# Kernel optimization log

Hardware: AMD Instinct MI355X
Metric: run time of the kernel (lower is better)

The kernel has to match this reference:

```python
import jax, jax.numpy as jnp
import numpy as np

N = 100000          # nodes
E = 1600000         # edges
D_NODE = 128        # num_node_features
D_EDGE = 128        # num_edge_features
OUT = 64            # out_features
HEADS = 2
HID = OUT * HEADS   # 128
NUM_GRAPHS = 64
NEG_SLOPE = 0.2


def setup_inputs() -> dict:
    key = jax.random.key(0)
    ks = jax.random.split(key, 12)
    glorot = lambda k, shape: jax.random.uniform(
        k, shape, jnp.float32, -1.0, 1.0) * np.sqrt(6.0 / (shape[0] + shape[-1]))
    return {
        "x": jax.random.normal(ks[0], (N, D_NODE), jnp.float32),
        "edge_index": jax.random.randint(ks[1], (2, E), 0, N, jnp.int64),
        "edge_attr": jax.random.normal(ks[2], (E, D_EDGE), jnp.float32),
        "batch": jnp.sort(jax.random.randint(ks[3], (N,), 0, NUM_GRAPHS, jnp.int64)),
        # GATConv params
        "lin_w": glorot(ks[4], (D_NODE, HID)),
        "att_src": glorot(ks[5], (HEADS, OUT)),
        "att_dst": glorot(ks[6], (HEADS, OUT)),
        "gat_bias": jnp.zeros((HID,), jnp.float32),
        # edge_lin params
        "edge_w": glorot(ks[7], (D_EDGE, HID)),
        "edge_b": jnp.zeros((HID,), jnp.float32),
        # MLP params
        "w1": glorot(ks[8], (HID, 32)),
        "b1": jnp.zeros((32,), jnp.float32),
        "w2": glorot(ks[9], (32, 1)),
        "b2": jnp.zeros((1,), jnp.float32),
    }


def reference(x, edge_index, edge_attr, batch, lin_w, att_src, att_dst,
              gat_bias, edge_w, edge_b, w1, b1, w2, b2):
    n = x.shape[0]
    # --- GATConv (concat=True, add_self_loops=True, negative_slope=0.2) ---
    h = (x @ lin_w).reshape(n, HEADS, OUT)                 # [N,H,C]
    loop = jnp.arange(n, dtype=edge_index.dtype)
    src = jnp.concatenate([edge_index[0], loop])           # [E+N]
    dst = jnp.concatenate([edge_index[1], loop])
    a_src = jnp.sum(h * att_src, axis=-1)                  # [N,H]
    a_dst = jnp.sum(h * att_dst, axis=-1)
    e = jax.nn.leaky_relu(a_src[src] + a_dst[dst], NEG_SLOPE)  # [E+N,H]
    e_max = jax.ops.segment_max(e, dst, num_segments=n)    # softmax over incoming edges
    e_exp = jnp.exp(e - e_max[dst])
    denom = jax.ops.segment_sum(e_exp, dst, num_segments=n)
    alpha = e_exp / (denom[dst] + 1e-16)                   # [E+N,H]
    msg = h[src] * alpha[:, :, None]                       # [E+N,H,C]
    node_feat = jax.ops.segment_sum(msg, dst, num_segments=n)
    node_feat = node_feat.reshape(n, HID) + gat_bias       # [N,HID]
    # --- edge features: linear + scatter-add to SOURCE node (the python loop) ---
    edge_feat = edge_attr @ edge_w + edge_b                # [E,HID]
    edge_agg = jax.ops.segment_sum(edge_feat, edge_index[0], num_segments=n)
    combined = node_feat + edge_agg                        # [N,HID]
    # --- global_add_pool + MLP ---
    pooled = jax.ops.segment_sum(combined, batch, num_segments=NUM_GRAPHS)
    return (pooled @ w1 + b1) @ w2 + b2                    # [NUM_GRAPHS,1]
```

## Files before the change

### kernel.cpp

```cpp
#include <hip/hip_runtime.h>
#include <hip/hip_bf16.h>
#include <math.h>


#define NG 64

__device__ __forceinline__ float lrelu(float v){ return v > 0.f ? v : 0.2f*v; }

__global__ __launch_bounds__(256) void k_zero(float4* __restrict__ p, long long n4,
                                              int* __restrict__ nstart)
{
  long long i = (long long)blockIdx.x*256 + threadIdx.x;
  long long stride = (long long)gridDim.x*256;
  float4 z = make_float4(0.f,0.f,0.f,0.f);
  for (; i < n4; i += stride) p[i] = z;
  if (blockIdx.x == 0 && threadIdx.x < NG) nstart[threadIdx.x] = 0x7fffffff;
}

__global__ __launch_bounds__(256) void k_gemm_h(
    const float* __restrict__ x, const float* __restrict__ W,
    const float* __restrict__ att_src, const float* __restrict__ att_dst,
    float* __restrict__ h, float* __restrict__ aS, float* __restrict__ aD,
    float* __restrict__ denom, int N)
{
  __shared__ float ldsX[32*128];
  int rb = blockIdx.x * 32;
  for (int idx = threadIdx.x; idx < 32*128/4; idx += 256){
    int k = (idx*4) & 127;
    int row = rb + (idx >> 5);
    float4 v = make_float4(0.f,0.f,0.f,0.f);
    if (row < N) v = *(const float4*)&x[(size_t)row*128 + k];
    *(float4*)&ldsX[idx*4] = v;
  }
  __syncthreads();
  int ty = threadIdx.x >> 5, tx = threadIdx.x & 31;
  int r0 = ty*4, c0 = tx*4;
  float acc[4][4] = {};
  #pragma unroll 4
  for (int k = 0; k < 128; ++k){
    float4 b = *(const float4*)&W[k*128 + c0];
    float a0 = ldsX[(r0+0)*128 + k];
    float a1 = ldsX[(r0+1)*128 + k];
    float a2 = ldsX[(r0+2)*128 + k];
    float a3 = ldsX[(r0+3)*128 + k];
    acc[0][0] += a0*b.x; acc[0][1] += a0*b.y; acc[0][2] += a0*b.z; acc[0][3] += a0*b.w;
    acc[1][0] += a1*b.x; acc[1][1] += a1*b.y; acc[1][2] += a1*b.z; acc[1][3] += a1*b.w;
    acc[2][0] += a2*b.x; acc[2][1] += a2*b.y; acc[2][2] += a2*b.z; acc[2][3] += a2*b.w;
    acc[3][0] += a3*b.x; acc[3][1] += a3*b.y; acc[3][2] += a3*b.z; acc[3][3] += a3*b.w;
  }
  #pragma unroll
  for (int i=0;i<4;++i){
    int row = rb + r0 + i;
    if (row < N){
      float4 v = make_float4(acc[i][0],acc[i][1],acc[i][2],acc[i][3]);
      *(float4*)&h[(size_t)row*128 + c0] = v;
    }
  }
  float4 vs = *(const float4*)&att_src[c0];
  float4 vd = *(const float4*)&att_dst[c0];
  int head = tx >> 4;
  #pragma unroll
  for (int i=0;i<4;++i){
    float ps = acc[i][0]*vs.x + acc[i][1]*vs.y + acc[i][2]*vs.z + acc[i][3]*vs.w;
    float pd = acc[i][0]*vd.x + acc[i][1]*vd.y + acc[i][2]*vd.z + acc[i][3]*vd.w;
    ps += __shfl_xor(ps,1); ps += __shfl_xor(ps,2); ps += __shfl_xor(ps,4); ps += __shfl_xor(ps,8);
    pd += __shfl_xor(pd,1); pd += __shfl_xor(pd,2); pd += __shfl_xor(pd,4); pd += __shfl_xor(pd,8);
    if ((tx & 15) == 0){
      int row = rb + r0 + i;
      if (row < N){
        aS[row*2+head] = ps;
        aD[row*2+head] = pd;
        denom[row*2+head] = __expf(lrelu(ps+pd));
      }
    }
  }
}

__global__ __launch_bounds__(256) void k_deg_denom(
  const int* __restrict__ src, const int* __restrict__ dst,
  const float* __restrict__ aS, const float* __restrict__ aD,
  int* __restrict__ deg, float* __restrict__ denom, int E)
{
  int e = blockIdx.x*256 + threadIdx.x; if (e >= E) return;
  int s = src[e], d = dst[e];
  atomicAdd(&deg[s], 1);
  float2 as = *(const float2*)&aS[(size_t)s*2];
  float2 ad = *(const float2*)&aD[(size_t)d*2];
  atomicAdd(&denom[d*2+0], __expf(lrelu(as.x+ad.x)));
  atomicAdd(&denom[d*2+1], __expf(lrelu(as.y+ad.y)));
}

__global__ __launch_bounds__(256) void k_bsum(
  const int* __restrict__ deg, int* __restrict__ bsum, int N)
{
  __shared__ int s[256];
  int b = blockIdx.x, t = threadIdx.x, base = b*1024;
  int sum = 0;
  #pragma unroll
  for (int q=0;q<4;++q){ int i = base + t*4 + q; if (i < N) sum += deg[i]; }
  s[t] = sum; __syncthreads();
  for (int o=128;o;o>>=1){ if (t<o) s[t]+=s[t+o]; __syncthreads(); }
  if (t==0) bsum[b] = s[0];
}

__global__ void k_bscan(const int* __restrict__ bsum, int* __restrict__ boff,
                        int* __restrict__ doff, int nbk, int N, int E)
{
  if (threadIdx.x == 0){
    int s = 0;
    for (int b=0;b<nbk;++b){ boff[b]=s; s+=bsum[b]; }
    doff[N] = E;
  }
}

__global__ __launch_bounds__(256) void k_doff(
  const int* __restrict__ deg, const int* __restrict__ boff,
  int* __restrict__ doff, int* __restrict__ gpos, int N)
{
  __shared__ int s[256];
  int b = blockIdx.x, t = threadIdx.x, base = b*1024;
  int v[4]; int t4 = 0;
  #pragma unroll
  for (int q=0;q<4;++q){ int i = base + t*4 + q; v[q] = (i<N)?deg[i]:0; t4 += v[q]; }
  s[t] = t4; __syncthreads();
  for (int o=1;o<256;o<<=1){
    int add = (t>=o)? s[t-o] : 0;
    __syncthreads();
    s[t] += add;
    __syncthreads();
  }
  int run = boff[b] + s[t] - t4;
  #pragma unroll
  for (int q=0;q<4;++q){
    int i = base + t*4 + q;
    if (i < N){ doff[i] = run; gpos[i] = run; run += v[q]; }
  }
}

__global__ __launch_bounds__(256) void k_node_post(
  const float* __restrict__ aD, const float* __restrict__ denom,
  const int* __restrict__ batch, float4* __restrict__ adn,
  int* __restrict__ nstart, int N)
{
  int i = blockIdx.x*256 + threadIdx.x; if (i >= N) return;
  adn[i] = make_float4(aD[i*2], aD[i*2+1], denom[i*2], denom[i*2+1]);
  int b = batch[i];
  if (i == 0 || batch[i-1] != b) atomicMin(&nstart[b], i);
}

__global__ void k_bounds(const int* __restrict__ nstart, const int* __restrict__ doff,
                         int N, int E, int* __restrict__ goff_e,
                         float* __restrict__ cnt_nf, float* __restrict__ cnt_ef)
{
  if (threadIdx.x != 0) return;
  int arr[NG+1];
  arr[NG] = N;
  for (int g=NG-1; g>=0; --g){
    int v = nstart[g];
    arr[g] = (v <= N) ? v : arr[g+1];
  }
  for (int g=0; g<NG; ++g) goff_e[g] = doff[arr[g]];
  goff_e[NG] = E;
  for (int g=0; g<NG; ++g){
    cnt_nf[g] = (float)(arr[g+1]-arr[g]);
    cnt_ef[g] = (float)(goff_e[g+1]-goff_e[g]);
  }
}

__global__ __launch_bounds__(256) void k_scatter(
  const int* __restrict__ src, const int* __restrict__ dst,
  int* __restrict__ gpos, int2* __restrict__ order2, int E)
{
  int e = blockIdx.x*256 + threadIdx.x; if (e >= E) return;
  int s = src[e];
  int p = atomicAdd(&gpos[s], 1);
  order2[p] = make_int2(e, dst[e] | ((s & 63) << 17));
}

__global__ __launch_bounds__(256) void k_alpha_rows(
  const int2* __restrict__ order2, const int* __restrict__ doff,
  const float* __restrict__ aS, const float4* __restrict__ adn,
  const int* __restrict__ batch, float* __restrict__ P, int N)
{
  __shared__ float row[64*128];
  __shared__ float saS[128];
  __shared__ int sb[64];
  int s0 = blockIdx.x*64, t = threadIdx.x;
  for (int idx=t; idx<2048; idx+=256) ((float4*)row)[idx] = make_float4(0,0,0,0);
  if (t < 128){ int i = s0*2 + t; saS[t] = (i < 2*N) ? aS[i] : 0.f; }
  if (t < 64){ int i = s0 + t; sb[t] = (i < N) ? batch[i] : 0; }
  __syncthreads();
  int hi = s0 + 64; if (hi > N) hi = N;
  int i0 = doff[s0], i1 = doff[hi];
  for (int i = i0 + t; i < i1; i += 256){
    int y = order2[i].y;
    int d = y & 0x1FFFF;
    int lo = (y >> 17) & 63;
    float4 q = adn[d];
    int gb = batch[d];
    float a0 = __expf(lrelu(saS[lo*2+0] + q.x)) / (q.z + 1e-16f);
    float a1 = __expf(lrelu(saS[lo*2+1] + q.y)) / (q.w + 1e-16f);
    atomicAdd(&row[lo*128 + gb],      a0);
    atomicAdd(&row[lo*128 + 64 + gb], a1);
  }
  __syncthreads();
  if (t < 64){
    int s = s0 + t;
    if (s < N){
      float4 q = adn[s];
      row[t*128 + sb[t]]      += __expf(lrelu(saS[t*2+0] + q.x)) / (q.z + 1e-16f);
      row[t*128 + 64 + sb[t]] += __expf(lrelu(saS[t*2+1] + q.y)) / (q.w + 1e-16f);
    }
  }
  __syncthreads();
  for (int idx=t; idx<2048; idx+=256){
    int r = idx >> 5;
    int s = s0 + r;
    if (s < N) ((float4*)&P[(size_t)s*128])[idx & 31] = ((float4*)row)[idx];
  }
}

__global__ __launch_bounds__(256) void k_pgemm(
  const float* __restrict__ P, const float* __restrict__ h,
  float* __restrict__ partial, int N)
{
  __shared__ float sP[64*128];
  int t = threadIdx.x;
  int c = t & 127;
  int gh = t >> 7;
  int head = c >> 6;
  float acc[32];
  #pragma unroll
  for (int i=0;i<32;++i) acc[i] = 0.f;
  int j0 = blockIdx.x * 256;
  for (int sbi=0; sbi<4; ++sbi){
    int jb = j0 + sbi*64;
    __syncthreads();
    for (int idx=t; idx<2048; idx+=256){
      int j = jb + (idx >> 5);
      ((float4*)sP)[idx] = (j < N) ? ((const float4*)&P[(size_t)j*128])[idx & 31]
                                   : make_float4(0,0,0,0);
    }
    __syncthreads();
    for (int jj=0; jj<64; ++jj){
      int j = jb + jj;
      float hv = (j < N) ? h[(size_t)j*128 + c] : 0.f;
      const float* rp = &sP[jj*128 + head*64 + gh*32];
      #pragma unroll
      for (int q=0;q<8;++q){
        float4 pv = *(const float4*)&rp[q*4];
        acc[q*4+0] += pv.x*hv; acc[q*4+1] += pv.y*hv;
        acc[q*4+2] += pv.z*hv; acc[q*4+3] += pv.w*hv;
      }
    }
  }
  float* pb = &partial[(size_t)blockIdx.x*8192];
  #pragma unroll
  for (int i=0;i<32;++i) pb[(gh*32+i)*128 + c] = acc[i];
}

__global__ __launch_bounds__(256) void k_pg_reduce(
  const float* __restrict__ partial, float* __restrict__ pooled_gat, int nPB)
{
  int o = blockIdx.x*256 + threadIdx.x;
  float s = 0.f;
  for (int b=0; b<nPB; ++b) s += partial[(size_t)b*8192 + o];
  pooled_gat[o] = s;
}

#define EA_SPLITS 64
__global__ __launch_bounds__(256) void k_eattr_sum(
  const float* __restrict__ ea, const int2* __restrict__ order2,
  const int* __restrict__ goff_e, float* __restrict__ pooled_e)
{
  __shared__ int sord[512];
  __shared__ float facc[128];
  int g = blockIdx.x / EA_SPLITS, k = blockIdx.x % EA_SPLITS;
  int start = goff_e[g], cnt = goff_e[g+1] - start;
  int len = (cnt + EA_SPLITS - 1) / EA_SPLITS;
  int i0 = start + k*len;
  int i1 = start + cnt; if (i0 + len < i1) i1 = i0 + len;
  int t = threadIdx.x, lane = t & 31, sub = t >> 5;
  const float4* ea4 = (const float4*)ea;
  float4 acc = make_float4(0.f,0.f,0.f,0.f);
  for (int base = i0; base < i1; base += 512){
    int m = i1 - base; if (m > 512) m = 512;
    __syncthreads();
    for (int idx = t; idx < m; idx += 256) sord[idx] = order2[base + idx].x;
    __syncthreads();
    int j = sub;
    for (; j + 56 < m; j += 64){
      float4 v0 = ea4[(size_t)sord[j     ]*32 + lane];
      float4 v1 = ea4[(size_t)sord[j +  8]*32 + lane];
      float4 v2 = ea4[(size_t)sord[j + 16]*32 + lane];
      float4 v3 = ea4[(size_t)sord[j + 24]*32 + lane];
      float4 v4 = ea4[(size_t)sord[j + 32]*32 + lane];
      float4 v5 = ea4[(size_t)sord[j + 40]*32 + lane];
      float4 v6 = ea4[(size_t)sord[j + 48]*32 + lane];
      float4 v7 = ea4[(size_t)sord[j + 56]*32 + lane];
      acc.x += (v0.x+v1.x)+(v2.x+v3.x)+((v4.x+v5.x)+(v6.x+v7.x));
      acc.y += (v0.y+v1.y)+(v2.y+v3.y)+((v4.y+v5.y)+(v6.y+v7.y));
      acc.z += (v0.z+v1.z)+(v2.z+v3.z)+((v4.z+v5.z)+(v6.z+v7.z));
      acc.w += (v0.w+v1.w)+(v2.w+v3.w)+((v4.w+v5.w)+(v6.w+v7.w));
    }
    for (; j < m; j += 8){
      float4 v = ea4[(size_t)sord[j]*32 + lane];
      acc.x += v.x; acc.y += v.y; acc.z += v.z; acc.w += v.w;
    }
  }
  if (t < 128) facc[t] = 0.f;
  __syncthreads();
  float* a = &facc[lane*4];
  atomicAdd(a+0, acc.x); atomicAdd(a+1, acc.y);
  atomicAdd(a+2, acc.z); atomicAdd(a+3, acc.w);
  __syncthreads();
  if (t < 128) atomicAdd(&pooled_e[g*128 + t], facc[t]);
}

__global__ __launch_bounds__(128) void k_final(
  const float* __restrict__ pooled_gat, const float* __restrict__ pooled_e,
  const float* __restrict__ cnt_nf, const float* __restrict__ cnt_ef,
  const float* __restrict__ gat_bias, const float* __restrict__ edge_w,
  const float* __restrict__ edge_b, const float* __restrict__ w1,
  const float* __restrict__ b1, const float* __restrict__ w2,
  const float* __restrict__ b2, float* __restrict__ out)
{
  __shared__ float lds_e[128], comb[128], t1[32];
  int g = blockIdx.x, c = threadIdx.x;
  lds_e[c] = pooled_e[g*128 + c];
  __syncthreads();
  float acc = pooled_gat[g*128 + c] + cnt_nf[g]*gat_bias[c] + cnt_ef[g]*edge_b[c];
  for (int k=0; k<128; ++k) acc += lds_e[k] * edge_w[k*128 + c];
  comb[c] = acc;
  __syncthreads();
  if (c < 32){
    float tv = b1[c];
    for (int k=0; k<128; ++k) tv += comb[k] * w1[k*32 + c];
    t1[c] = tv;
  }
  __syncthreads();
  if (c == 0){
    float o = b2[0];
    #pragma unroll
    for (int m=0; m<32; ++m) o += t1[m] * w2[m];
    out[g] = o;
  }
}

extern "C" void kernel_launch(void* const* d_in, const int* in_sizes, int n_in,
                              void* d_out, int out_size, void* d_ws, size_t ws_size,
                              hipStream_t stream) {
  const float* x        = (const float*)d_in[0];
  const int*   ei       = (const int*)d_in[1];
  const float* ea       = (const float*)d_in[2];
  const int*   batch    = (const int*)d_in[3];
  const float* lin_w    = (const float*)d_in[4];
  const float* att_src  = (const float*)d_in[5];
  const float* att_dst  = (const float*)d_in[6];
  const float* gat_bias = (const float*)d_in[7];
  const float* edge_w   = (const float*)d_in[8];
  const float* edge_b   = (const float*)d_in[9];
  const float* w1       = (const float*)d_in[10];
  const float* b1       = (const float*)d_in[11];
  const float* w2       = (const float*)d_in[12];
  const float* b2       = (const float*)d_in[13];
  float* out = (float*)d_out;

  int N = in_sizes[0] / 128;
  int E = in_sizes[1] / 2;
  const int* src = ei;
  const int* dst = ei + E;
  int nbk = (N + 1023) / 1024;
  int nPB = (N + 255) / 256;

  char* ws = (char*)d_ws;
  size_t off = 0;
  float* pooled_e   = (float*)(ws + off); off += (size_t)NG*128*4;
  int*   deg        = (int*)  (ws + off); off += ((size_t)N*4 + 15) & ~15ull;
  size_t zero_bytes = off;
  float* pooled_gat = (float*)(ws + off); off += (size_t)NG*128*4;
  float* h        = (float*)(ws + off); off += (size_t)N*128*4;
  float* P        = (float*)(ws + off); off += (size_t)N*128*4;
  float* partial  = (float*)(ws + off); off += (size_t)nPB*8192*4;
  float* aS       = (float*)(ws + off); off += (size_t)2*N*4;
  float* aD       = (float*)(ws + off); off += (size_t)2*N*4;
  float* denom    = (float*)(ws + off); off += (size_t)2*N*4;
  float4* adn     = (float4*)(ws + off); off += (size_t)N*16;
  int*   doff     = (int*)  (ws + off); off += ((size_t)(N+1)*4 + 15) & ~15ull;
  int*   gpos     = (int*)  (ws + off); off += ((size_t)N*4 + 15) & ~15ull;
  int2*  order2   = (int2*) (ws + off); off += (size_t)E*8;
  int*   bsum     = (int*)  (ws + off); off += 1024*4;
  int*   boff     = (int*)  (ws + off); off += 1024*4;
  int*   nstart   = (int*)  (ws + off); off += NG*4;
  int*   goff_e   = (int*)  (ws + off); off += (NG+1)*4;
  float* cnt_nf   = (float*)(ws + off); off += NG*4;
  float* cnt_ef   = (float*)(ws + off); off += NG*4;

  k_zero<<<128, 256, 0, stream>>>((float4*)d_ws, (long long)(zero_bytes/16), nstart);

  k_gemm_h   <<<(N+31)/32, 256, 0, stream>>>(x, lin_w, att_src, att_dst,
                                             h, aS, aD, denom, N);
  k_deg_denom<<<(E+255)/256, 256, 0, stream>>>(src, dst, aS, aD, deg, denom, E);

  k_bsum     <<<nbk, 256, 0, stream>>>(deg, bsum, N);
  k_bscan    <<<1, 1, 0, stream>>>(bsum, boff, doff, nbk, N, E);
  k_doff     <<<nbk, 256, 0, stream>>>(deg, boff, doff, gpos, N);
  k_node_post<<<(N+255)/256, 256, 0, stream>>>(aD, denom, batch, adn, nstart, N);
  k_bounds   <<<1, 1, 0, stream>>>(nstart, doff, N, E, goff_e, cnt_nf, cnt_ef);
  k_scatter  <<<(E+255)/256, 256, 0, stream>>>(src, dst, gpos, order2, E);

  k_alpha_rows<<<(N+63)/64, 256, 0, stream>>>(order2, doff, aS, adn, batch, P, N);
  k_pgemm     <<<nPB, 256, 0, stream>>>(P, h, partial, N);
  k_pg_reduce <<<32, 256, 0, stream>>>(partial, pooled_gat, nPB);

  k_eattr_sum<<<NG*EA_SPLITS, 256, 0, stream>>>(ea, order2, goff_e, pooled_e);

  k_final<<<NG, 128, 0, stream>>>(pooled_gat, pooled_e, cnt_nf, cnt_ef,
                                  gat_bias, edge_w, edge_b, w1, b1, w2, b2, out);
}
```

Baseline: 822.2 us.

## Split edge order into SoA arrays, pack batch id, retune pgemm and reduction

The interleaved int2 edge-order buffer becomes two separate int arrays, so the alpha and edge-attribute passes each read only the field they use. The destination's graph id is packed into the order word at scatter time, which removes a random batch[] gather in k_alpha_rows. k_pgemm now covers 128 nodes per block instead of 256, giving more blocks and more parallelism, and the partial-sum reduction is split across a 2D grid that combines results with atomics into a pre-zeroed pooled_gat. The price is a doubled partial buffer that the reduce must read, plus atomic contention during the final combine.

```diff
diff --git a/kernel.cpp b/kernel.cpp
--- a/kernel.cpp
+++ b/kernel.cpp
@@ -169,16 +169,19 @@
 
 __global__ __launch_bounds__(256) void k_scatter(
   const int* __restrict__ src, const int* __restrict__ dst,
-  int* __restrict__ gpos, int2* __restrict__ order2, int E)
+  const int* __restrict__ batch, int* __restrict__ gpos,
+  int* __restrict__ order_x, int* __restrict__ order_y, int E)
 {
   int e = blockIdx.x*256 + threadIdx.x; if (e >= E) return;
-  int s = src[e];
+  int s = src[e], d = dst[e];
+  int gb = batch[d];
   int p = atomicAdd(&gpos[s], 1);
-  order2[p] = make_int2(e, dst[e] | ((s & 63) << 17));
+  order_x[p] = e;
+  order_y[p] = d | ((s & 63) << 17) | (gb << 23);
 }
 
 __global__ __launch_bounds__(256) void k_alpha_rows(
-  const int2* __restrict__ order2, const int* __restrict__ doff,
+  const int* __restrict__ order_y, const int* __restrict__ doff,
   const float* __restrict__ aS, const float4* __restrict__ adn,
   const int* __restrict__ batch, float* __restrict__ P, int N)
 {
@@ -193,11 +196,11 @@
   int hi = s0 + 64; if (hi > N) hi = N;
   int i0 = doff[s0], i1 = doff[hi];
   for (int i = i0 + t; i < i1; i += 256){
-    int y = order2[i].y;
+    int y = order_y[i];
     int d = y & 0x1FFFF;
     int lo = (y >> 17) & 63;
+    int gb = (y >> 23) & 63;
     float4 q = adn[d];
-    int gb = batch[d];
     float a0 = __expf(lrelu(saS[lo*2+0] + q.x)) / (q.z + 1e-16f);
     float a1 = __expf(lrelu(saS[lo*2+1] + q.y)) / (q.w + 1e-16f);
     atomicAdd(&row[lo*128 + gb],      a0);
@@ -232,8 +235,8 @@
   float acc[32];
   #pragma unroll
   for (int i=0;i<32;++i) acc[i] = 0.f;
-  int j0 = blockIdx.x * 256;
-  for (int sbi=0; sbi<4; ++sbi){
+  int j0 = blockIdx.x * 128;
+  for (int sbi=0; sbi<2; ++sbi){
     int jb = j0 + sbi*64;
     __syncthreads();
     for (int idx=t; idx<2048; idx+=256){
@@ -263,14 +266,17 @@
   const float* __restrict__ partial, float* __restrict__ pooled_gat, int nPB)
 {
   int o = blockIdx.x*256 + threadIdx.x;
+  int chunk = (nPB + gridDim.y - 1) / gridDim.y;
+  int b0 = blockIdx.y * chunk;
+  int b1 = b0 + chunk; if (b1 > nPB) b1 = nPB;
   float s = 0.f;
-  for (int b=0; b<nPB; ++b) s += partial[(size_t)b*8192 + o];
-  pooled_gat[o] = s;
+  for (int b=b0; b<b1; ++b) s += partial[(size_t)b*8192 + o];
+  atomicAdd(&pooled_gat[o], s);
 }
 
 #define EA_SPLITS 64
 __global__ __launch_bounds__(256) void k_eattr_sum(
-  const float* __restrict__ ea, const int2* __restrict__ order2,
+  const float* __restrict__ ea, const int* __restrict__ order_x,
   const int* __restrict__ goff_e, float* __restrict__ pooled_e)
 {
   __shared__ int sord[512];
@@ -286,7 +292,7 @@
   for (int base = i0; base < i1; base += 512){
     int m = i1 - base; if (m > 512) m = 512;
     __syncthreads();
-    for (int idx = t; idx < m; idx += 256) sord[idx] = order2[base + idx].x;
+    for (int idx = t; idx < m; idx += 256) sord[idx] = order_x[base + idx];
     __syncthreads();
     int j = sub;
     for (; j + 56 < m; j += 64){
@@ -371,14 +377,14 @@
   const int* src = ei;
   const int* dst = ei + E;
   int nbk = (N + 1023) / 1024;
-  int nPB = (N + 255) / 256;
+  int nPB = (N + 127) / 128;
 
   char* ws = (char*)d_ws;
   size_t off = 0;
   float* pooled_e   = (float*)(ws + off); off += (size_t)NG*128*4;
+  float* pooled_gat = (float*)(ws + off); off += (size_t)NG*128*4;
   int*   deg        = (int*)  (ws + off); off += ((size_t)N*4 + 15) & ~15ull;
   size_t zero_bytes = off;
-  float* pooled_gat = (float*)(ws + off); off += (size_t)NG*128*4;
   float* h        = (float*)(ws + off); off += (size_t)N*128*4;
   float* P        = (float*)(ws + off); off += (size_t)N*128*4;
   float* partial  = (float*)(ws + off); off += (size_t)nPB*8192*4;
@@ -388,7 +394,8 @@
   float4* adn     = (float4*)(ws + off); off += (size_t)N*16;
   int*   doff     = (int*)  (ws + off); off += ((size_t)(N+1)*4 + 15) & ~15ull;
   int*   gpos     = (int*)  (ws + off); off += ((size_t)N*4 + 15) & ~15ull;
-  int2*  order2   = (int2*) (ws + off); off += (size_t)E*8;
+  int*   order_x  = (int*)  (ws + off); off += (size_t)E*4;
+  int*   order_y  = (int*)  (ws + off); off += (size_t)E*4;
   int*   bsum     = (int*)  (ws + off); off += 1024*4;
   int*   boff     = (int*)  (ws + off); off += 1024*4;
   int*   nstart   = (int*)  (ws + off); off += NG*4;
@@ -407,13 +414,17 @@
   k_doff     <<<nbk, 256, 0, stream>>>(deg, boff, doff, gpos, N);
   k_node_post<<<(N+255)/256, 256, 0, stream>>>(aD, denom, batch, adn, nstart, N);
   k_bounds   <<<1, 1, 0, stream>>>(nstart, doff, N, E, goff_e, cnt_nf, cnt_ef);
-  k_scatter  <<<(E+255)/256, 256, 0, stream>>>(src, dst, gpos, order2, E);
-
-  k_alpha_rows<<<(N+63)/64, 256, 0, stream>>>(order2, doff, aS, adn, batch, P, N);
+  k_scatter  <<<(E+255)/256, 256, 0, stream>>>(src, dst, batch, gpos,
+                                               order_x, order_y, E);
+
+  k_alpha_rows<<<(N+63)/64, 256, 0, stream>>>(order_y, doff, aS, adn, batch, P, N);
   k_pgemm     <<<nPB, 256, 0, stream>>>(P, h, partial, N);
-  k_pg_reduce <<<32, 256, 0, stream>>>(partial, pooled_gat, nPB);
-
-  k_eattr_sum<<<NG*EA_SPLITS, 256, 0, stream>>>(ea, order2, goff_e, pooled_e);
+  {
+    dim3 rg(32, 8);
+    k_pg_reduce<<<rg, 256, 0, stream>>>(partial, pooled_gat, nPB);
+  }
+
+  k_eattr_sum<<<NG*EA_SPLITS, 256, 0, stream>>>(ea, order_x, goff_e, pooled_e);
 
   k_final<<<NG, 128, 0, stream>>>(pooled_gat, pooled_e, cnt_nf, cnt_ef,
                                   gat_bias, edge_w, edge_b, w1, b1, w2, b2, out);
```

Measured after the change: 737.0 us. -10.4%, faster.
